# Performance work log

Hardware: AMD Instinct MI355X
Metric: run time of the kernel (lower is better)

## Reference

```python
import jax, jax.numpy as jnp
import numpy as np

NQ = 9  # 9 qubits per 3x3 patch; state shape (M, 2,...,2), axis (NQ-q) holds qubit q (qiskit little-endian)

def _ax(q):
    return NQ - q

def _bcast(theta):
    theta = jnp.asarray(theta)
    if theta.ndim == 1:  # per-patch angle -> broadcast over 8 remaining qubit axes
        return theta.reshape((-1,) + (1,) * (NQ - 1))
    return theta

def apply_1q(state, q, m00, m01, m10, m11):
    ax = _ax(q)
    s0 = jnp.take(state, 0, axis=ax)
    s1 = jnp.take(state, 1, axis=ax)
    return jnp.stack([m00 * s0 + m01 * s1, m10 * s0 + m11 * s1], axis=ax)

def apply_ry(state, q, theta):
    th = _bcast(theta) * 0.5
    c = jnp.cos(th).astype(state.dtype)
    s = jnp.sin(th).astype(state.dtype)
    return apply_1q(state, q, c, -s, s, c)

def apply_rz(state, q, theta):
    th = _bcast(theta) * 0.5
    e = jnp.exp(-1j * th.astype(jnp.complex64))
    return apply_1q(state, q, e, 0.0, 0.0, jnp.conj(e))

def apply_cx(state, c, t):
    axc, axt = _ax(c), _ax(t)
    sc0 = jnp.take(state, 0, axis=axc)
    sc1 = jnp.take(state, 1, axis=axc)
    axt2 = axt - 1 if axt > axc else axt
    sc1 = jnp.flip(sc1, axis=axt2)  # X on target within control=1 subspace
    return jnp.stack([sc0, sc1], axis=axc)

def apply_crx(state, c, t, theta):
    axc, axt = _ax(c), _ax(t)
    sc0 = jnp.take(state, 0, axis=axc)
    sc1 = jnp.take(state, 1, axis=axc)
    axt2 = axt - 1 if axt > axc else axt
    t0 = jnp.take(sc1, 0, axis=axt2)
    t1 = jnp.take(sc1, 1, axis=axt2)
    co = jnp.cos(theta * 0.5)
    si = jnp.sin(theta * 0.5)
    sc1 = jnp.stack([co * t0 - 1j * si * t1, -1j * si * t0 + co * t1], axis=axt2)
    return jnp.stack([sc0, sc1], axis=axc)

def qcnn_batched(angles, w):
    """angles: (M, 9) input rotation angles. w: (42,) shared weights. Returns (M, 3) = [<X>,<Y>,<Z>] on qubit 0."""
    M = angles.shape[0]
    state = jnp.zeros((M,) + (2,) * NQ, dtype=jnp.complex64)
    state = state.at[(slice(None),) + (0,) * NQ].set(1.0)
    for q in range(NQ):  # input encoding
        state = apply_ry(state, q, angles[:, q])
    wi = 0
    # conv1: RY + RZ on all 9 qubits, ring CNOT
    for q in range(NQ):
        state = apply_ry(state, q, w[wi]); wi += 1
    for q in range(NQ):
        state = apply_rz(state, q, w[wi]); wi += 1
    for i in range(NQ):
        state = apply_cx(state, i, (i + 1) % NQ)
    # pool1: 6 CRX gates
    for (c, t) in [(1, 0), (2, 0), (4, 3), (5, 3), (7, 6), (8, 6)]:
        state = apply_crx(state, c, t, w[wi]); wi += 1
    # conv2 on qubits [0,3,6]
    for q in [0, 3, 6]:
        state = apply_ry(state, q, w[wi]); wi += 1
    for q in [0, 3, 6]:
        state = apply_rz(state, q, w[wi]); wi += 1
    for (c, t) in [(0, 3), (3, 6), (6, 0)]:
        state = apply_cx(state, c, t)
    state = apply_ry(state, 0, w[wi])
    state = apply_rz(state, 3, w[wi + 1]); wi += 2
    # pool2
    state = apply_crx(state, 3, 0, w[wi])
    state = apply_crx(state, 3, 6, w[wi + 1])
    state = apply_ry(state, 0, w[wi + 2])
    state = apply_ry(state, 6, w[wi + 3]); wi += 4
    # conv3
    state = apply_ry(state, 0, w[wi])
    state = apply_ry(state, 6, w[wi + 1])
    state = apply_cx(state, 0, 6)
    state = apply_rz(state, 0, w[wi + 2])
    state = apply_rz(state, 6, w[wi + 3]); wi += 4
    # pool3
    state = apply_crx(state, 6, 0, w[wi])
    state = apply_ry(state, 0, w[wi + 1]); wi += 2
    assert wi == 42
    # expectations <X>,<Y>,<Z> on qubit 0 (last axis)
    a0 = jnp.take(state, 0, axis=NQ)
    a1 = jnp.take(state, 1, axis=NQ)
    axes = tuple(range(1, NQ))
    z = jnp.sum(jnp.conj(a0) * a1, axis=axes)
    ex = 2.0 * jnp.real(z)
    ey = 2.0 * jnp.imag(z)
    ez = jnp.sum(jnp.abs(a0) ** 2 - jnp.abs(a1) ** 2, axis=axes)
    return jnp.stack([ex, ey, ez], axis=-1).astype(jnp.float32)

def setup_inputs() -> dict:
    key = jax.random.key(0)
    k1, k2, k3 = jax.random.split(key, 3)
    B, H, WS, NCLS = 8, 28, 3, 10
    n = H - WS + 1  # 26 patches per side
    x = jax.random.uniform(k1, (B, 1, H, H), dtype=jnp.float32)
    w = jax.random.normal(k2, (42,), dtype=jnp.float32)
    fc_w = jax.random.normal(k3, (NCLS, n * n * 3), dtype=jnp.float32) * 0.02
    fc_b = jnp.zeros((NCLS,), dtype=jnp.float32)
    return {"x": x, "w": w, "fc_w": fc_w, "fc_b": fc_b}

def reference(x, w, fc_w, fc_b):
    B, H, WS = x.shape[0], x.shape[2], 3
    n = H - WS + 1
    # extract 3x3 patches, row-major within window (matches torch unfold+view)
    patches = jnp.stack([x[:, 0, i:i + n, j:j + n] for i in range(WS) for j in range(WS)], axis=-1)  # (B,n,n,9)
    angles = patches.reshape(B * n * n, WS * WS) * jnp.pi
    bloch = qcnn_batched(angles, w)  # (B*N, 3)
    feats = bloch.reshape(B, n * n * 3)  # patch-major [X,Y,Z] per patch, matches torch.cat over patches
    return feats @ fc_w.T + fc_b
```

## Files before the change

kernel.cpp:

```cpp
#include <hip/hip_runtime.h>


__device__ __forceinline__ float shx(float v, int m) { return __shfl_xor(v, m, 64); }

__device__ __forceinline__ float2 cmul(float2 a, float2 b) {
  return make_float2(a.x * b.x - a.y * b.y, a.x * b.y + a.y * b.x);
}

template <int TM> __device__ __forceinline__
void ry_r(float (&re)[8], float (&im)[8], float c, float s) {
#pragma unroll
  for (int r0 = 0; r0 < 8; ++r0) if (!(r0 & TM)) {
    const int r1 = r0 | TM;
    float a = re[r0], bb = re[r1];
    re[r0] = c * a - s * bb; re[r1] = s * a + c * bb;
    a = im[r0]; bb = im[r1];
    im[r0] = c * a - s * bb; im[r1] = s * a + c * bb;
  }
}
template <int TM> __device__ __forceinline__
void rz_r(float (&re)[8], float (&im)[8], float c, float s) {
#pragma unroll
  for (int r = 0; r < 8; ++r) {
    const float sg = (r & TM) ? s : -s;
    const float a = re[r], bb = im[r];
    re[r] = c * a - sg * bb;
    im[r] = c * bb + sg * a;
  }
}
template <int CM, int TM> __device__ __forceinline__
void cx_rr(float (&re)[8], float (&im)[8]) {
#pragma unroll
  for (int r0 = 0; r0 < 8; ++r0) if ((r0 & CM) && !(r0 & TM)) {
    const int r1 = r0 | TM;
    float t = re[r0]; re[r0] = re[r1]; re[r1] = t;
    t = im[r0]; im[r0] = im[r1]; im[r1] = t;
  }
}
template <int CM, int TM> __device__ __forceinline__
void crx_rr(float (&re)[8], float (&im)[8], float co, float si) {
#pragma unroll
  for (int r0 = 0; r0 < 8; ++r0) if ((r0 & CM) && !(r0 & TM)) {
    const int r1 = r0 | TM;
    const float r0r = re[r0], r0i = im[r0], r1r = re[r1], r1i = im[r1];
    re[r0] = co * r0r + si * r1i; im[r0] = co * r0i - si * r1r;
    re[r1] = co * r1r + si * r0i; im[r1] = co * r1i - si * r0r;
  }
}

__device__ __forceinline__
void ry_f(float2& A, float2& B, float c, float s) {
  const float2 nA = make_float2(c * A.x - s * B.x, c * A.y - s * B.y);
  const float2 nB = make_float2(s * A.x + c * B.x, s * A.y + c * B.y);
  A = nA; B = nB;
}
__device__ __forceinline__
void rz_f(float2& A, float2& B, float c, float s) {
  A = make_float2(c * A.x + s * A.y, c * A.y - s * A.x);
  B = make_float2(c * B.x - s * B.y, c * B.y + s * B.x);
}
__device__ __forceinline__
void rx_f(float2& A, float2& B, float c, float s) {
  const float2 nA = make_float2(c * A.x + s * B.y, c * A.y - s * B.x);
  const float2 nB = make_float2(c * B.x + s * A.y, c * B.y - s * A.x);
  A = nA; B = nB;
}

__global__ __launch_bounds__(256) void qcnn_fused(const float* __restrict__ x,
                                                  const float* __restrict__ w,
                                                  float* __restrict__ feats) {
  __shared__ float4 tauT[4][9];
  __shared__ float2 rxT[4][12];
  __shared__ float2 gT[4][16];

  const int tid = threadIdx.x;
  const int wv = tid >> 6, lane = tid & 63;
  const unsigned p = blockIdx.x * 4u + wv;
  const unsigned b = p / 676u;
  const unsigned rem = p - b * 676u;
  const unsigned i = rem / 26u, j = rem - i * 26u;

  if (lane < 9) {
    const int di = lane / 3, dj = lane - di * 3;
    const float xv = x[b * 784u + (i + di) * 28u + (j + dj)];
    const float ang = fmaf(xv, 3.14159265358979323846f, w[lane]) * 0.5f;
    float s, c; __sincosf(ang, &s, &c);
    float zs, zc; __sincosf(0.5f * w[9 + lane], &zs, &zc);
    tauT[wv][lane] = make_float4(c * zc, -c * zs, s * zc, s * zs);
  } else if (lane < 21) {
    const int k = lane - 9, a = k >> 2, cb = k & 3;
    float th = 0.0f;
    if (cb & 1) th += w[18 + 2 * a];
    if (cb & 2) th += w[19 + 2 * a];
    float s, c; __sincosf(0.5f * th, &s, &c);
    rxT[wv][k] = make_float2(c, s);
  } else if (lane < 37) {
    const int k = lane - 21;
    float th;
    if (k < 10)       th = w[24 + k];
    else if (k == 10) th = w[34] + w[36];
    else if (k == 11) th = w[35] + w[37];
    else              th = w[26 + k];
    float s, c; __sincosf(0.5f * th, &s, &c);
    gT[wv][k] = make_float2(c, s);
  }

  const int l0 = lane & 1, l1 = (lane >> 1) & 1, l2 = (lane >> 2) & 1;
  const int l3 = (lane >> 3) & 1, l4 = (lane >> 4) & 1, l5 = (lane >> 5) & 1;

  float4 tq[9];
#pragma unroll
  for (int q = 0; q < 9; ++q) tq[q] = tauT[wv][q];
  auto tau = [&](int bit, int q) -> float2 {
    const float4 t = tq[q];
    return bit ? make_float2(t.z, t.w) : make_float2(t.x, t.y);
  };

  const int a0 = l5, a1 = l0 ^ l5;
  float2 p00 = cmul(tau(a0, 0), tau(a1, 1));
  float2 p01 = cmul(tau(a0 ^ 1, 0), tau(a1 ^ 1, 1));
  float2 p10 = cmul(tau(l1, 3), tau(l2, 4));
  float2 p11 = cmul(tau(l1 ^ 1, 3), tau(l2 ^ 1, 4));
  float2 p20 = cmul(tau(l3, 6), tau(l4, 7));
  float2 p21 = cmul(tau(l3 ^ 1, 6), tau(l4 ^ 1, 7));
  const float2 T = cmul(cmul(tau(l0 ^ l1, 2), tau(l2 ^ l3, 5)), tau(l4 ^ l5, 8));
  p20 = cmul(p20, T);
  p21 = cmul(p21, T);

  {
    const float2 x0 = rxT[wv][lane & 3];
    const float2 x1 = rxT[wv][4 + ((lane >> 2) & 3)];
    const float2 x2 = rxT[wv][8 + ((lane >> 4) & 3)];
    rx_f(p00, p01, x0.x, x0.y);
    rx_f(p10, p11, x1.x, x1.y);
    rx_f(p20, p21, x2.x, x2.y);
  }

  {
    const float2 g0 = gT[wv][0], g1 = gT[wv][1], g2 = gT[wv][2];
    const float2 g3 = gT[wv][3], g4 = gT[wv][4], g5 = gT[wv][5];
    ry_f(p00, p01, g0.x, g0.y);
    ry_f(p10, p11, g1.x, g1.y);
    ry_f(p20, p21, g2.x, g2.y);
    rz_f(p00, p01, g3.x, g3.y);
    rz_f(p10, p11, g4.x, g4.y);
    rz_f(p20, p21, g5.x, g5.y);
  }

  float re[8], im[8];
  {
    const float2 q00 = cmul(p00, p10);
    const float2 q01 = cmul(p00, p11);
    const float2 q10 = cmul(p01, p10);
    const float2 q11 = cmul(p01, p11);
    float2 u;
    u = cmul(q00, p20); re[0] = u.x; im[0] = u.y;
    u = cmul(q11, p20); re[1] = u.x; im[1] = u.y;
    u = cmul(q01, p21); re[2] = u.x; im[2] = u.y;
    u = cmul(q10, p21); re[3] = u.x; im[3] = u.y;
    u = cmul(q11, p21); re[4] = u.x; im[4] = u.y;
    u = cmul(q00, p21); re[5] = u.x; im[5] = u.y;
    u = cmul(q10, p20); re[6] = u.x; im[6] = u.y;
    u = cmul(q01, p20); re[7] = u.x; im[7] = u.y;
  }

  {
    const float2 g6 = gT[wv][6],  g7 = gT[wv][7],  g8 = gT[wv][8];
    const float2 g9 = gT[wv][9],  gA = gT[wv][10], gB = gT[wv][11];
    const float2 gC = gT[wv][12], gD = gT[wv][13], gE = gT[wv][14];
    const float2 gF = gT[wv][15];
    ry_r<1>(re, im, g6.x, g6.y);
    rz_r<2>(re, im, g7.x, g7.y);
    crx_rr<2, 1>(re, im, g8.x, g8.y);
    crx_rr<2, 4>(re, im, g9.x, g9.y);
    ry_r<1>(re, im, gA.x, gA.y);
    ry_r<4>(re, im, gB.x, gB.y);
    cx_rr<1, 4>(re, im);
    rz_r<1>(re, im, gC.x, gC.y);
    rz_r<4>(re, im, gD.x, gD.y);
    crx_rr<4, 1>(re, im, gE.x, gE.y);
    ry_r<1>(re, im, gF.x, gF.y);
  }

  float zr = 0.f, zi = 0.f, pe = 0.f;
#pragma unroll
  for (int r0 = 0; r0 < 8; r0 += 2) {
    const int r1 = r0 + 1;
    zr += re[r0] * re[r1] + im[r0] * im[r1];
    zi += re[r0] * im[r1] - im[r0] * re[r1];
    pe += re[r0] * re[r0] + im[r0] * im[r0];
  }
#pragma unroll
  for (int m = 1; m < 64; m <<= 1) { zr += shx(zr, m); zi += shx(zi, m); pe += shx(pe, m); }

  if (lane == 0) {
    feats[p * 3u + 0u] = 2.0f * zr;
    feats[p * 3u + 1u] = 2.0f * zi;
    feats[p * 3u + 2u] = 2.0f * pe - 1.0f;
  }
}

__global__ __launch_bounds__(256) void fc_kernel(const float* __restrict__ feats,
                                                 const float* __restrict__ fc_w,
                                                 const float* __restrict__ fc_b,
                                                 float* __restrict__ out) {
  const int b = blockIdx.x / 10, c = blockIdx.x - b * 10;
  const float* f = feats + b * 2028;
  const float* wr = fc_w + c * 2028;
  float acc = 0.0f;
  for (int k = threadIdx.x; k < 2028; k += 256) acc += f[k] * wr[k];
#pragma unroll
  for (int m = 1; m < 64; m <<= 1) acc += __shfl_xor(acc, m, 64);
  __shared__ float sbuf[4];
  const int lane = threadIdx.x & 63, wv = threadIdx.x >> 6;
  if (lane == 0) sbuf[wv] = acc;
  __syncthreads();
  if (threadIdx.x == 0) out[b * 10 + c] = sbuf[0] + sbuf[1] + sbuf[2] + sbuf[3] + fc_b[c];
}

extern "C" void kernel_launch(void* const* d_in, const int* in_sizes, int n_in,
                              void* d_out, int out_size, void* d_ws, size_t ws_size,
                              hipStream_t stream) {
  const float* x    = (const float*)d_in[0];
  const float* w    = (const float*)d_in[1];
  const float* fc_w = (const float*)d_in[2];
  const float* fc_b = (const float*)d_in[3];
  float* out = (float*)d_out;

  const int B = in_sizes[0] / 784;
  const int npatch = B * 676;

  float* feats = (float*)d_ws;

  qcnn_fused<<<npatch / 4, 256, 0, stream>>>(x, w, feats);
  fc_kernel<<<B * 10, 256, 0, stream>>>(feats, fc_w, fc_b, out);
}
```

Measured before the change: 68.65 us.

## Fuse FC layer into QCNN kernel using per-block partial dot products and atomics

Removes the separate fc_kernel and the feats workspace round-trip. Each block writes its four patches' Bloch features to shared memory, and ten threads compute partial dot products against the matching 12 fc_w columns, then atomically add them into the output. The bias is added once by the first block of each batch row. The output is zeroed with a memset beforehand, which adds a memset launch plus about 16k atomics in place of the second kernel launch.

```diff
diff --git a/kernel.cpp b/kernel.cpp
--- a/kernel.cpp
+++ b/kernel.cpp
@@ -68,10 +68,13 @@
 
 __global__ __launch_bounds__(256) void qcnn_fused(const float* __restrict__ x,
                                                   const float* __restrict__ w,
-                                                  float* __restrict__ feats) {
+                                                  const float* __restrict__ fc_w,
+                                                  const float* __restrict__ fc_b,
+                                                  float* __restrict__ out) {
   __shared__ float4 tauT[4][9];
   __shared__ float2 rxT[4][12];
   __shared__ float2 gT[4][16];
+  __shared__ float sfeat[12];
 
   const int tid = threadIdx.x;
   const int wv = tid >> 6, lane = tid & 63;
@@ -194,28 +197,25 @@
   for (int m = 1; m < 64; m <<= 1) { zr += shx(zr, m); zi += shx(zi, m); pe += shx(pe, m); }
 
   if (lane == 0) {
-    feats[p * 3u + 0u] = 2.0f * zr;
-    feats[p * 3u + 1u] = 2.0f * zi;
-    feats[p * 3u + 2u] = 2.0f * pe - 1.0f;
-  }
-}
-
-__global__ __launch_bounds__(256) void fc_kernel(const float* __restrict__ feats,
-                                                 const float* __restrict__ fc_w,
-                                                 const float* __restrict__ fc_b,
-                                                 float* __restrict__ out) {
-  const int b = blockIdx.x / 10, c = blockIdx.x - b * 10;
-  const float* f = feats + b * 2028;
-  const float* wr = fc_w + c * 2028;
-  float acc = 0.0f;
-  for (int k = threadIdx.x; k < 2028; k += 256) acc += f[k] * wr[k];
-#pragma unroll
-  for (int m = 1; m < 64; m <<= 1) acc += __shfl_xor(acc, m, 64);
-  __shared__ float sbuf[4];
-  const int lane = threadIdx.x & 63, wv = threadIdx.x >> 6;
-  if (lane == 0) sbuf[wv] = acc;
+    sfeat[wv * 3 + 0] = 2.0f * zr;
+    sfeat[wv * 3 + 1] = 2.0f * zi;
+    sfeat[wv * 3 + 2] = 2.0f * pe - 1.0f;
+  }
+
   __syncthreads();
-  if (threadIdx.x == 0) out[b * 10 + c] = sbuf[0] + sbuf[1] + sbuf[2] + sbuf[3] + fc_b[c];
+  if (tid < 10) {
+    const int c = tid;
+    const unsigned bb = blockIdx.x / 169u;
+    const unsigned lb = blockIdx.x - bb * 169u;
+    const unsigned base_col = lb * 12u;
+    const float4* wp = reinterpret_cast<const float4*>(fc_w + c * 2028u + base_col);
+    const float4 w0 = wp[0], w1 = wp[1], w2 = wp[2];
+    float acc = w0.x * sfeat[0] + w0.y * sfeat[1] + w0.z * sfeat[2] + w0.w * sfeat[3];
+    acc      += w1.x * sfeat[4] + w1.y * sfeat[5] + w1.z * sfeat[6] + w1.w * sfeat[7];
+    acc      += w2.x * sfeat[8] + w2.y * sfeat[9] + w2.z * sfeat[10] + w2.w * sfeat[11];
+    if (lb == 0) acc += fc_b[c];
+    atomicAdd(&out[bb * 10u + c], acc);
+  }
 }
 
 extern "C" void kernel_launch(void* const* d_in, const int* in_sizes, int n_in,
@@ -230,8 +230,6 @@
   const int B = in_sizes[0] / 784;
   const int npatch = B * 676;
 
-  float* feats = (float*)d_ws;
-
-  qcnn_fused<<<npatch / 4, 256, 0, stream>>>(x, w, feats);
-  fc_kernel<<<B * 10, 256, 0, stream>>>(feats, fc_w, fc_b, out);
-}
+  hipMemsetAsync(out, 0, (size_t)(B * 10) * sizeof(float), stream);
+  qcnn_fused<<<npatch / 4, 256, 0, stream>>>(x, w, fc_w, fc_b, out);
+}
```

After: 76.28 us. +11.1%, slower.
